# Performance work log

Measured on AMD Instinct MI355X. Metric: run time of the kernel, lower is better.

## Reference

```python
import jax, jax.numpy as jnp
import numpy as np

B, T, D_MODEL, HEAD_DIM = 4, 4096, 1024, 64

def setup_inputs() -> dict:
    key = jax.random.key(0)
    ks = jax.random.split(key, 7)
    s = 1.0 / np.sqrt(D_MODEL)
    return {
        "x": jax.random.normal(ks[0], (B, T, D_MODEL), dtype=jnp.float32),
        "Wq": jax.random.uniform(ks[1], (D_MODEL, HEAD_DIM), jnp.float32, -s, s),
        "bq": jax.random.uniform(ks[2], (HEAD_DIM,), jnp.float32, -s, s),
        "Wk": jax.random.uniform(ks[3], (D_MODEL, HEAD_DIM), jnp.float32, -s, s),
        "bk": jax.random.uniform(ks[4], (HEAD_DIM,), jnp.float32, -s, s),
        "Wv": jax.random.uniform(ks[5], (D_MODEL, HEAD_DIM), jnp.float32, -s, s),
        "bv": jax.random.uniform(ks[6], (HEAD_DIM,), jnp.float32, -s, s),
    }

def reference(x, Wq, bq, Wk, bk, Wv, bv):
    # x: [B,T,D]; projections -> [B,T,H]
    q = jnp.einsum("btd,dh->bth", x, Wq) + bq
    k = jnp.einsum("btd,dh->bth", x, Wk) + bk
    v = jnp.einsum("btd,dh->bth", x, Wv) + bv
    scale = HEAD_DIM ** -0.5
    # scores: [B,Tq,Tk] -- naive full attention matrix (memory-bound)
    scores = jnp.einsum("bqh,bkh->bqk", q, k) * scale
    neg = jnp.finfo(scores.dtype).min
    T_ = scores.shape[-1]
    causal = jnp.triu(jnp.full((T_, T_), neg, dtype=scores.dtype), k=1)
    scores = scores + causal[None, :, :]
    probs = jax.nn.softmax(scores, axis=-1)
    y = jnp.einsum("bqk,bkh->bqh", probs, v)
    return y
```

## Files before the change

kernel.cpp:

```cpp
#include <hip/hip_runtime.h>
#include <hip/hip_bf16.h>

typedef __attribute__((ext_vector_type(4))) float f4v;
typedef __attribute__((ext_vector_type(16))) float f16v;
typedef __attribute__((ext_vector_type(4))) unsigned short u16x4;
typedef __attribute__((ext_vector_type(8))) unsigned short u16x8;
typedef __attribute__((ext_vector_type(2))) unsigned int u32x2;
typedef __attribute__((ext_vector_type(4))) unsigned int u32x4;
typedef __attribute__((ext_vector_type(8))) __bf16 bf16x8;

#define D_MODEL 1024
#define HDIM 64
#define TSEQ 4096
#define QB 32
#define KVB 64
#define QSCALE 0.18033688011112042f

__device__ __forceinline__ unsigned short f2bf(float f) {
    union { float f; unsigned u; } v; v.f = f;
    unsigned r = v.u + 0x7FFFu + ((v.u >> 16) & 1u);
    return (unsigned short)(r >> 16);
}
__device__ __forceinline__ float asf(unsigned u) {
    union { unsigned u; float f; } v; v.u = u; return v.f;
}
__device__ __forceinline__ bf16x8 ld8(const unsigned short* p) {
    return __builtin_bit_cast(bf16x8, *(const u16x8*)p);
}
__device__ __forceinline__ f4v mfma16(bf16x8 a, bf16x8 b, f4v c) {
    return __builtin_amdgcn_mfma_f32_16x16x32_bf16(a, b, c, 0, 0, 0);
}
__device__ __forceinline__ f16v mfma32(bf16x8 a, bf16x8 b, f16v c) {
    return __builtin_amdgcn_mfma_f32_32x32x16_bf16(a, b, c, 0, 0, 0);
}
__device__ __forceinline__ unsigned cvtpk(float a, float b) {
    unsigned r;
    asm("v_cvt_pk_bf16_f32 %0, %1, %2" : "=v"(r) : "v"(a), "v"(b));
    return r;
}
__device__ __forceinline__ void pswap(unsigned& a, unsigned& b) {
    asm("v_permlane32_swap_b32 %0, %1" : "+v"(a), "+v"(b));
}

__global__ void prep_wf(const float* __restrict__ Wq, const float* __restrict__ Wk,
                        const float* __restrict__ Wv, unsigned short* __restrict__ Wf)
{
    int idx = blockIdx.x * 256 + threadIdx.x;
    int j = idx & 7, lane = (idx >> 3) & 63, nf = (idx >> 9) & 3,
        kstep = (idx >> 11) & 31, m = idx >> 16;
    int k = kstep * 32 + 8 * (lane >> 4) + j;
    int n = nf * 16 + (lane & 15);
    const float* W = (m == 0) ? Wq : (m == 1) ? Wk : Wv;
    Wf[idx] = f2bf(W[k * 64 + n]);
}

__global__ __launch_bounds__(256, 2)
void proj_qkv(const float* __restrict__ x, const unsigned short* __restrict__ Wf,
              const float* __restrict__ bq, const float* __restrict__ bk,
              const float* __restrict__ bv,
              unsigned short* __restrict__ Qf, unsigned short* __restrict__ Kf,
              unsigned short* __restrict__ Vf)
{
    __shared__ unsigned short xhi[32][72];
    __shared__ unsigned short xlo[32][72];

    const int tid = threadIdx.x;
    const int w = tid >> 6, l = tid & 63;
    const int row0 = blockIdx.x * 32;

    f4v acc[2][3];
#pragma unroll
    for (int s = 0; s < 2; ++s)
#pragma unroll
        for (int f = 0; f < 3; ++f) acc[s][f] = (f4v)0.f;

    for (int k0 = 0; k0 < D_MODEL; k0 += 64) {
        __syncthreads();
#pragma unroll
        for (int io = 0; io < 2; ++io) {
            int id = io * 256 + tid;
            int r = id >> 4, c4 = id & 15;
            f4v a = *(const f4v*)(x + (size_t)(row0 + r) * D_MODEL + k0 + c4 * 4);
            unsigned p0 = cvtpk(a[0], a[1]), p1 = cvtpk(a[2], a[3]);
            u32x2 hw = {p0, p1};
            *(u16x4*)&xhi[r][c4 * 4] = __builtin_bit_cast(u16x4, hw);
            float e0 = a[0] - asf(p0 << 16), e1 = a[1] - asf(p0 & 0xFFFF0000u);
            float e2 = a[2] - asf(p1 << 16), e3 = a[3] - asf(p1 & 0xFFFF0000u);
            unsigned q0 = cvtpk(e0, e1), q1 = cvtpk(e2, e3);
            u32x2 lw = {q0, q1};
            *(u16x4*)&xlo[r][c4 * 4] = __builtin_bit_cast(u16x4, lw);
        }
        __syncthreads();
#pragma unroll
        for (int ks = 0; ks < 2; ++ks) {
            const int kglob = (k0 >> 5) + ks;
            bf16x8 bw[3];
#pragma unroll
            for (int f = 0; f < 3; ++f) {
                const int cf = w * 3 + f;
                bw[f] = ld8(Wf + ((((cf >> 2) * 32 + kglob) * 4 + (cf & 3)) << 9) + l * 8);
            }
#pragma unroll
            for (int s = 0; s < 2; ++s) {
                bf16x8 xh = ld8(&xhi[s * 16 + (l & 15)][ks * 32 + 8 * (l >> 4)]);
                bf16x8 xl = ld8(&xlo[s * 16 + (l & 15)][ks * 32 + 8 * (l >> 4)]);
#pragma unroll
                for (int f = 0; f < 3; ++f) {
                    acc[s][f] = mfma16(xh, bw[f], acc[s][f]);
                    acc[s][f] = mfma16(xl, bw[f], acc[s][f]);
                }
            }
        }
    }

    const float* bias[3] = {bq, bk, bv};
#pragma unroll
    for (int s = 0; s < 2; ++s) {
        const int rowb = row0 + s * 16 + 4 * (l >> 4);
        const int b = rowb >> 12, tok0 = rowb & 4095;
#pragma unroll
        for (int f = 0; f < 3; ++f) {
            const int cf = w * 3 + f;
            const int m = cf >> 2, nf = cf & 3;
            const int d = nf * 16 + (l & 15);
            const float bb = bias[m][d];
            if (m == 0) {
                const int qtile = tok0 >> 5;
                const int ksq = d >> 4, hq = (d >> 3) & 1, jq = d & 7;
#pragma unroll
                for (int r4 = 0; r4 < 4; ++r4) {
                    int cq = (tok0 & 31) + r4;
                    Qf[(((size_t)(b * 128 + qtile) * 4 + ksq) << 9) + (32 * hq + cq) * 8 + jq] =
                        f2bf((acc[s][f][r4] + bb) * QSCALE);
                }
            } else if (m == 1) {
                const int t = tok0 >> 6, tb = (tok0 >> 5) & 1;
                const int ksk = d >> 4, hk = (d >> 3) & 1, jk = d & 7;
#pragma unroll
                for (int r4 = 0; r4 < 4; ++r4) {
                    int ck = (tok0 & 31) + r4;
                    Kf[(((size_t)((b * 64 + t) * 8 + tb * 4 + ksk)) << 9) + (32 * hk + ck) * 8 + jk] =
                        f2bf(acc[s][f][r4] + bb);
                }
            } else {
                const int t = tok0 >> 6, ku = (tok0 >> 4) & 3, hv = (tok0 >> 3) & 1, jv = tok0 & 7;
                const int cv = d & 31, td = d >> 5;
                u16x4 pk;
#pragma unroll
                for (int r4 = 0; r4 < 4; ++r4) pk[r4] = f2bf(acc[s][f][r4] + bb);
                *(u16x4*)(Vf + (((size_t)((b * 64 + t) * 8 + td * 4 + ku)) << 9) +
                          (32 * hv + cv) * 8 + jv) = pk;
            }
        }
    }
}

struct TState { float m, l; f16v o0, o1; };

__device__ __forceinline__ void run_tile(const unsigned short* __restrict__ Qf,
                                         const unsigned short* __restrict__ Kf,
                                         const unsigned short* __restrict__ Vf,
                                         int batch, int qt, int g8, int l, int h, int c,
                                         TState& st)
{
    const int NT = (qt >> 1) + 1;
    st.m = -1e30f; st.l = 0.f; st.o0 = (f16v)0.f; st.o1 = (f16v)0.f;

    bf16x8 qf[4];
    const unsigned short* qp = Qf + (((size_t)(batch * 128 + qt) * 4) << 9) + l * 8;
#pragma unroll
    for (int ks = 0; ks < 4; ++ks) qf[ks] = ld8(qp + (ks << 9));

    if (g8 >= NT) return;

    auto kload = [&](bf16x8(&kr)[2][4], int t_) {
        const unsigned short* p = Kf + (((size_t)(batch * 64 + t_) * 8) << 9) + l * 8;
#pragma unroll
        for (int tb = 0; tb < 2; ++tb)
#pragma unroll
            for (int ks = 0; ks < 4; ++ks)
                kr[tb][ks] = ld8(p + ((tb * 4 + ks) << 9));
    };

    auto body = [&](bf16x8(&kr)[2][4], bf16x8(&kn)[2][4], int t_) {
        bf16x8 vr[2][4];
        {
            const unsigned short* p = Vf + (((size_t)(batch * 64 + t_) * 8) << 9) + l * 8;
#pragma unroll
            for (int td = 0; td < 2; ++td)
#pragma unroll
                for (int ku = 0; ku < 4; ++ku)
                    vr[td][ku] = ld8(p + ((td * 4 + ku) << 9));
        }
        f16v sacc[2];
        sacc[0] = (f16v)0.f; sacc[1] = (f16v)0.f;
#pragma unroll
        for (int ks = 0; ks < 4; ++ks) {
            sacc[0] = mfma32(kr[0][ks], qf[ks], sacc[0]);
            sacc[1] = mfma32(kr[1][ks], qf[ks], sacc[1]);
        }
        int tn = t_ + 8; if (tn > NT - 1) tn = NT - 1;
        kload(kn, tn);
        if (t_ == NT - 1) {
            const int off = qt * QB - t_ * KVB;
#pragma unroll
            for (int tb = 0; tb < 2; ++tb)
#pragma unroll
                for (int r = 0; r < 16; ++r) {
                    int mv = 32 * tb + (r & 3) + 8 * (r >> 2) + 4 * h - off;
                    if (mv > c) sacc[tb][r] = -1e30f;
                }
        }
        float pm = -1e30f;
#pragma unroll
        for (int tb = 0; tb < 2; ++tb)
#pragma unroll
            for (int r = 0; r < 16; ++r) pm = fmaxf(pm, sacc[tb][r]);
        pm = fmaxf(pm, __shfl_xor(pm, 32));
        const float mnew = fmaxf(st.m, pm);
        const float sc = exp2f(st.m - mnew);
        st.m = mnew;
        float rs = 0.f;
        float p[2][16];
#pragma unroll
        for (int tb = 0; tb < 2; ++tb)
#pragma unroll
            for (int r = 0; r < 16; ++r) {
                float e = exp2f(sacc[tb][r] - mnew);
                p[tb][r] = e; rs += e;
            }
        rs += __shfl_xor(rs, 32);
        st.l = st.l * sc + rs;
#pragma unroll
        for (int r = 0; r < 16; ++r) { st.o0[r] *= sc; st.o1[r] *= sc; }
        bf16x8 pa[4];
#pragma unroll
        for (int tb = 0; tb < 2; ++tb) {
            unsigned wp[8];
#pragma unroll
            for (int i = 0; i < 8; ++i) wp[i] = cvtpk(p[tb][2 * i], p[tb][2 * i + 1]);
            pswap(wp[0], wp[2]); pswap(wp[1], wp[3]);
            pswap(wp[4], wp[6]); pswap(wp[5], wp[7]);
            u32x4 f0 = {wp[0], wp[1], wp[2], wp[3]};
            u32x4 f1 = {wp[4], wp[5], wp[6], wp[7]};
            pa[2 * tb]     = __builtin_bit_cast(bf16x8, f0);
            pa[2 * tb + 1] = __builtin_bit_cast(bf16x8, f1);
        }
#pragma unroll
        for (int ku = 0; ku < 4; ++ku) {
            st.o0 = mfma32(vr[0][ku], pa[ku], st.o0);
            st.o1 = mfma32(vr[1][ku], pa[ku], st.o1);
        }
    };

    bf16x8 kA[2][4], kB[2][4];
    int t = g8;
    kload(kA, t);
    for (;;) {
        body(kA, kB, t);
        t += 8; if (t >= NT) break;
        body(kB, kA, t);
        t += 8; if (t >= NT) break;
    }
}

__global__ __launch_bounds__(512, 2)
void attn(const unsigned short* __restrict__ Qf, const unsigned short* __restrict__ Kf,
          const unsigned short* __restrict__ Vf, float* __restrict__ Yg)
{
    __shared__ float Osm[8][QB][33];
    __shared__ float Msm[2][8][QB];
    __shared__ float Lsm[2][8][QB];

    const int tid = threadIdx.x;
    const int g8 = tid >> 6, l = tid & 63, h = l >> 5, c = l & 31;
    const int batch = blockIdx.x & 3;
    const int pr = blockIdx.x >> 2;
    const int qtA = pr, qtB = 127 - pr;

    TState sB, sA;
    run_tile(Qf, Kf, Vf, batch, qtB, g8, l, h, c, sB);
    run_tile(Qf, Kf, Vf, batch, qtA, g8, l, h, c, sA);

    if (h == 0) {
        Msm[0][g8][c] = sA.m; Lsm[0][g8][c] = sA.l;
        Msm[1][g8][c] = sB.m; Lsm[1][g8][c] = sB.l;
    }

    auto write_partial = [&](const f16v& o) {
#pragma unroll
        for (int r = 0; r < 16; ++r) {
            int dd = (r & 3) + 8 * (r >> 2) + 4 * h;
            Osm[g8][c][dd] = o[r];
        }
    };
    auto merge_phase = [&](int tile, int dhalf, int qt_) {
        const int q = tid >> 4, d2 = (tid & 15) * 2;
        float mm = -1e30f;
#pragma unroll
        for (int gg = 0; gg < 8; ++gg) mm = fmaxf(mm, Msm[tile][gg][q]);
        float L = 0.f, o0 = 0.f, o1 = 0.f;
#pragma unroll
        for (int gg = 0; gg < 8; ++gg) {
            float a = exp2f(Msm[tile][gg][q] - mm);
            L += a * Lsm[tile][gg][q];
            o0 += a * Osm[gg][q][d2];
            o1 += a * Osm[gg][q][d2 + 1];
        }
        float inv = 1.f / L;
        float* yp = Yg + ((size_t)batch * TSEQ + (size_t)qt_ * QB + q) * HDIM + dhalf * 32 + d2;
        yp[0] = o0 * inv; yp[1] = o1 * inv;
    };

    write_partial(sA.o0);
    __syncthreads();
    merge_phase(0, 0, qtA);
    __syncthreads();
    write_partial(sA.o1);
    __syncthreads();
    merge_phase(0, 1, qtA);
    __syncthreads();
    write_partial(sB.o0);
    __syncthreads();
    merge_phase(1, 0, qtB);
    __syncthreads();
    write_partial(sB.o1);
    __syncthreads();
    merge_phase(1, 1, qtB);
}

extern "C" void kernel_launch(void* const* d_in, const int* in_sizes, int n_in,
                              void* d_out, int out_size, void* d_ws, size_t ws_size,
                              hipStream_t stream)
{
    const float* x  = (const float*)d_in[0];
    const float* Wq = (const float*)d_in[1];
    const float* bq = (const float*)d_in[2];
    const float* Wk = (const float*)d_in[3];
    const float* bk = (const float*)d_in[4];
    const float* Wv = (const float*)d_in[5];
    const float* bv = (const float*)d_in[6];
    float* y = (float*)d_out;

    unsigned short* Qb = (unsigned short*)d_ws;
    unsigned short* Kb = Qb + (size_t)1048576;
    unsigned short* Vb = Kb + (size_t)1048576;
    unsigned short* Wf = Vb + (size_t)1048576;

    prep_wf<<<768, 256, 0, stream>>>(Wq, Wk, Wv, Wf);
    proj_qkv<<<512, 256, 0, stream>>>(x, Wf, bq, bk, bv, Qb, Kb, Vb);
    attn<<<256, 512, 0, stream>>>(Qb, Kb, Vb, y);
}
```

Before: 56.76 us.

## Halve projection row tile, double-buffer x staging with register prefetch

```diff
diff --git a/kernel.cpp b/kernel.cpp
--- a/kernel.cpp
+++ b/kernel.cpp
@@ -54,103 +54,94 @@
     Wf[idx] = f2bf(W[k * 64 + n]);
 }
 
-__global__ __launch_bounds__(256, 2)
+__global__ __launch_bounds__(256, 4)
 void proj_qkv(const float* __restrict__ x, const unsigned short* __restrict__ Wf,
               const float* __restrict__ bq, const float* __restrict__ bk,
               const float* __restrict__ bv,
               unsigned short* __restrict__ Qf, unsigned short* __restrict__ Kf,
               unsigned short* __restrict__ Vf)
 {
-    __shared__ unsigned short xhi[32][72];
-    __shared__ unsigned short xlo[32][72];
+    __shared__ unsigned short xhi[2][16][72];
+    __shared__ unsigned short xlo[2][16][72];
 
     const int tid = threadIdx.x;
     const int w = tid >> 6, l = tid & 63;
-    const int row0 = blockIdx.x * 32;
-
-    f4v acc[2][3];
-#pragma unroll
-    for (int s = 0; s < 2; ++s)
-#pragma unroll
-        for (int f = 0; f < 3; ++f) acc[s][f] = (f4v)0.f;
-
-    for (int k0 = 0; k0 < D_MODEL; k0 += 64) {
+    const int row0 = blockIdx.x * 16;
+    const int sr = tid >> 4, sc = tid & 15;
+    const float* xp = x + (size_t)(row0 + sr) * D_MODEL + sc * 4;
+
+    f4v acc[3];
+#pragma unroll
+    for (int f = 0; f < 3; ++f) acc[f] = (f4v)0.f;
+
+    f4v xv = *(const f4v*)xp;
+
+#pragma unroll
+    for (int t = 0; t < 16; ++t) {
+        unsigned p0 = cvtpk(xv[0], xv[1]), p1 = cvtpk(xv[2], xv[3]);
+        u32x2 hw = {p0, p1};
+        *(u16x4*)&xhi[t & 1][sr][sc * 4] = __builtin_bit_cast(u16x4, hw);
+        float e0 = xv[0] - asf(p0 << 16), e1 = xv[1] - asf(p0 & 0xFFFF0000u);
+        float e2 = xv[2] - asf(p1 << 16), e3 = xv[3] - asf(p1 & 0xFFFF0000u);
+        unsigned q0 = cvtpk(e0, e1), q1 = cvtpk(e2, e3);
+        u32x2 lw = {q0, q1};
+        *(u16x4*)&xlo[t & 1][sr][sc * 4] = __builtin_bit_cast(u16x4, lw);
+        if (t < 15) xv = *(const f4v*)(xp + 64 * (t + 1));
         __syncthreads();
 #pragma unroll
-        for (int io = 0; io < 2; ++io) {
-            int id = io * 256 + tid;
-            int r = id >> 4, c4 = id & 15;
-            f4v a = *(const f4v*)(x + (size_t)(row0 + r) * D_MODEL + k0 + c4 * 4);
-            unsigned p0 = cvtpk(a[0], a[1]), p1 = cvtpk(a[2], a[3]);
-            u32x2 hw = {p0, p1};
-            *(u16x4*)&xhi[r][c4 * 4] = __builtin_bit_cast(u16x4, hw);
-            float e0 = a[0] - asf(p0 << 16), e1 = a[1] - asf(p0 & 0xFFFF0000u);
-            float e2 = a[2] - asf(p1 << 16), e3 = a[3] - asf(p1 & 0xFFFF0000u);
-            unsigned q0 = cvtpk(e0, e1), q1 = cvtpk(e2, e3);
-            u32x2 lw = {q0, q1};
-            *(u16x4*)&xlo[r][c4 * 4] = __builtin_bit_cast(u16x4, lw);
-        }
-        __syncthreads();
-#pragma unroll
         for (int ks = 0; ks < 2; ++ks) {
-            const int kglob = (k0 >> 5) + ks;
+            const int kglob = t * 2 + ks;
             bf16x8 bw[3];
 #pragma unroll
             for (int f = 0; f < 3; ++f) {
                 const int cf = w * 3 + f;
                 bw[f] = ld8(Wf + ((((cf >> 2) * 32 + kglob) * 4 + (cf & 3)) << 9) + l * 8);
             }
-#pragma unroll
-            for (int s = 0; s < 2; ++s) {
-                bf16x8 xh = ld8(&xhi[s * 16 + (l & 15)][ks * 32 + 8 * (l >> 4)]);
-                bf16x8 xl = ld8(&xlo[s * 16 + (l & 15)][ks * 32 + 8 * (l >> 4)]);
-#pragma unroll
-                for (int f = 0; f < 3; ++f) {
-                    acc[s][f] = mfma16(xh, bw[f], acc[s][f]);
-                    acc[s][f] = mfma16(xl, bw[f], acc[s][f]);
-                }
+            bf16x8 xh = ld8(&xhi[t & 1][l & 15][ks * 32 + 8 * (l >> 4)]);
+            bf16x8 xl = ld8(&xlo[t & 1][l & 15][ks * 32 + 8 * (l >> 4)]);
+#pragma unroll
+            for (int f = 0; f < 3; ++f) {
+                acc[f] = mfma16(xh, bw[f], acc[f]);
+                acc[f] = mfma16(xl, bw[f], acc[f]);
             }
         }
     }
 
     const float* bias[3] = {bq, bk, bv};
-#pragma unroll
-    for (int s = 0; s < 2; ++s) {
-        const int rowb = row0 + s * 16 + 4 * (l >> 4);
-        const int b = rowb >> 12, tok0 = rowb & 4095;
-#pragma unroll
-        for (int f = 0; f < 3; ++f) {
-            const int cf = w * 3 + f;
-            const int m = cf >> 2, nf = cf & 3;
-            const int d = nf * 16 + (l & 15);
-            const float bb = bias[m][d];
-            if (m == 0) {
-                const int qtile = tok0 >> 5;
-                const int ksq = d >> 4, hq = (d >> 3) & 1, jq = d & 7;
-#pragma unroll
-                for (int r4 = 0; r4 < 4; ++r4) {
-                    int cq = (tok0 & 31) + r4;
-                    Qf[(((size_t)(b * 128 + qtile) * 4 + ksq) << 9) + (32 * hq + cq) * 8 + jq] =
-                        f2bf((acc[s][f][r4] + bb) * QSCALE);
-                }
-            } else if (m == 1) {
-                const int t = tok0 >> 6, tb = (tok0 >> 5) & 1;
-                const int ksk = d >> 4, hk = (d >> 3) & 1, jk = d & 7;
-#pragma unroll
-                for (int r4 = 0; r4 < 4; ++r4) {
-                    int ck = (tok0 & 31) + r4;
-                    Kf[(((size_t)((b * 64 + t) * 8 + tb * 4 + ksk)) << 9) + (32 * hk + ck) * 8 + jk] =
-                        f2bf(acc[s][f][r4] + bb);
-                }
-            } else {
-                const int t = tok0 >> 6, ku = (tok0 >> 4) & 3, hv = (tok0 >> 3) & 1, jv = tok0 & 7;
-                const int cv = d & 31, td = d >> 5;
-                u16x4 pk;
-#pragma unroll
-                for (int r4 = 0; r4 < 4; ++r4) pk[r4] = f2bf(acc[s][f][r4] + bb);
-                *(u16x4*)(Vf + (((size_t)((b * 64 + t) * 8 + td * 4 + ku)) << 9) +
-                          (32 * hv + cv) * 8 + jv) = pk;
-            }
+    const int rowb = row0 + 4 * (l >> 4);
+    const int b = rowb >> 12, tok0 = rowb & 4095;
+#pragma unroll
+    for (int f = 0; f < 3; ++f) {
+        const int cf = w * 3 + f;
+        const int m = cf >> 2, nf = cf & 3;
+        const int d = nf * 16 + (l & 15);
+        const float bb = bias[m][d];
+        if (m == 0) {
+            const int qtile = tok0 >> 5;
+            const int ksq = d >> 4, hq = (d >> 3) & 1, jq = d & 7;
+#pragma unroll
+            for (int r4 = 0; r4 < 4; ++r4) {
+                int cq = (tok0 & 31) + r4;
+                Qf[(((size_t)(b * 128 + qtile) * 4 + ksq) << 9) + (32 * hq + cq) * 8 + jq] =
+                    f2bf((acc[f][r4] + bb) * QSCALE);
+            }
+        } else if (m == 1) {
+            const int t = tok0 >> 6, tb = (tok0 >> 5) & 1;
+            const int ksk = d >> 4, hk = (d >> 3) & 1, jk = d & 7;
+#pragma unroll
+            for (int r4 = 0; r4 < 4; ++r4) {
+                int ck = (tok0 & 31) + r4;
+                Kf[(((size_t)((b * 64 + t) * 8 + tb * 4 + ksk)) << 9) + (32 * hk + ck) * 8 + jk] =
+                    f2bf(acc[f][r4] + bb);
+            }
+        } else {
+            const int t = tok0 >> 6, ku = (tok0 >> 4) & 3, hv = (tok0 >> 3) & 1, jv = tok0 & 7;
+            const int cv = d & 31, td = d >> 5;
+            u16x4 pk;
+#pragma unroll
+            for (int r4 = 0; r4 < 4; ++r4) pk[r4] = f2bf(acc[f][r4] + bb);
+            *(u16x4*)(Vf + (((size_t)((b * 64 + t) * 8 + td * 4 + ku)) << 9) +
+                      (32 * hv + cv) * 8 + jv) = pk;
         }
     }
 }
@@ -348,6 +339,6 @@
     unsigned short* Wf = Vb + (size_t)1048576;
 
     prep_wf<<<768, 256, 0, stream>>>(Wq, Wk, Wv, Wf);
-    proj_qkv<<<512, 256, 0, stream>>>(x, Wf, bq, bk, bv, Qb, Kb, Vb);
+    proj_qkv<<<1024, 256, 0, stream>>>(x, Wf, bq, bk, bv, Qb, Kb, Vb);
     attn<<<256, 512, 0, stream>>>(Qb, Kb, Vb, y);
 }
```

Result: faster. 51.80 us (-8.7%).

## Switch QKV projection to fp16 MFMA with async double-buffered LDS staging

Applied to the files above, without the earlier changes.

```diff
diff --git a/kernel.cpp b/kernel.cpp
--- a/kernel.cpp
+++ b/kernel.cpp
@@ -8,6 +8,7 @@
 typedef __attribute__((ext_vector_type(2))) unsigned int u32x2;
 typedef __attribute__((ext_vector_type(4))) unsigned int u32x4;
 typedef __attribute__((ext_vector_type(8))) __bf16 bf16x8;
+typedef __attribute__((ext_vector_type(8))) _Float16 h8v;
 
 #define D_MODEL 1024
 #define HDIM 64
@@ -21,14 +22,14 @@
     unsigned r = v.u + 0x7FFFu + ((v.u >> 16) & 1u);
     return (unsigned short)(r >> 16);
 }
-__device__ __forceinline__ float asf(unsigned u) {
-    union { unsigned u; float f; } v; v.u = u; return v.f;
-}
 __device__ __forceinline__ bf16x8 ld8(const unsigned short* p) {
     return __builtin_bit_cast(bf16x8, *(const u16x8*)p);
 }
-__device__ __forceinline__ f4v mfma16(bf16x8 a, bf16x8 b, f4v c) {
-    return __builtin_amdgcn_mfma_f32_16x16x32_bf16(a, b, c, 0, 0, 0);
+__device__ __forceinline__ h8v ldh8(const unsigned short* p) {
+    return __builtin_bit_cast(h8v, *(const u16x8*)p);
+}
+__device__ __forceinline__ f4v mfma16f(h8v a, h8v b, f4v c) {
+    return __builtin_amdgcn_mfma_f32_16x16x32_f16(a, b, c, 0, 0, 0);
 }
 __device__ __forceinline__ f16v mfma32(bf16x8 a, bf16x8 b, f16v c) {
     return __builtin_amdgcn_mfma_f32_32x32x16_bf16(a, b, c, 0, 0, 0);
@@ -40,6 +41,14 @@
 }
 __device__ __forceinline__ void pswap(unsigned& a, unsigned& b) {
     asm("v_permlane32_swap_b32 %0, %1" : "+v"(a), "+v"(b));
+}
+__device__ __forceinline__ h8v pack8(f4v a, f4v b) {
+    unsigned p0 = __builtin_bit_cast(unsigned, __builtin_amdgcn_cvt_pkrtz(a[0], a[1]));
+    unsigned p1 = __builtin_bit_cast(unsigned, __builtin_amdgcn_cvt_pkrtz(a[2], a[3]));
+    unsigned p2 = __builtin_bit_cast(unsigned, __builtin_amdgcn_cvt_pkrtz(b[0], b[1]));
+    unsigned p3 = __builtin_bit_cast(unsigned, __builtin_amdgcn_cvt_pkrtz(b[2], b[3]));
+    u32x4 u = {p0, p1, p2, p3};
+    return __builtin_bit_cast(h8v, u);
 }
 
 __global__ void prep_wf(const float* __restrict__ Wq, const float* __restrict__ Wk,
@@ -51,7 +60,8 @@
     int k = kstep * 32 + 8 * (lane >> 4) + j;
     int n = nf * 16 + (lane & 15);
     const float* W = (m == 0) ? Wq : (m == 1) ? Wk : Wv;
-    Wf[idx] = f2bf(W[k * 64 + n]);
+    _Float16 hv = (_Float16)W[k * 64 + n];
+    Wf[idx] = __builtin_bit_cast(unsigned short, hv);
 }
 
 __global__ __launch_bounds__(256, 2)
@@ -61,8 +71,7 @@
               unsigned short* __restrict__ Qf, unsigned short* __restrict__ Kf,
               unsigned short* __restrict__ Vf)
 {
-    __shared__ unsigned short xhi[32][72];
-    __shared__ unsigned short xlo[32][72];
+    __shared__ float xs[2][4096];
 
     const int tid = threadIdx.x;
     const int w = tid >> 6, l = tid & 63;
@@ -74,43 +83,51 @@
 #pragma unroll
         for (int f = 0; f < 3; ++f) acc[s][f] = (f4v)0.f;
 
-    for (int k0 = 0; k0 < D_MODEL; k0 += 64) {
-        __syncthreads();
-#pragma unroll
-        for (int io = 0; io < 2; ++io) {
-            int id = io * 256 + tid;
-            int r = id >> 4, c4 = id & 15;
-            f4v a = *(const f4v*)(x + (size_t)(row0 + r) * D_MODEL + k0 + c4 * 4);
-            unsigned p0 = cvtpk(a[0], a[1]), p1 = cvtpk(a[2], a[3]);
-            u32x2 hw = {p0, p1};
-            *(u16x4*)&xhi[r][c4 * 4] = __builtin_bit_cast(u16x4, hw);
-            float e0 = a[0] - asf(p0 << 16), e1 = a[1] - asf(p0 & 0xFFFF0000u);
-            float e2 = a[2] - asf(p1 << 16), e3 = a[3] - asf(p1 & 0xFFFF0000u);
-            unsigned q0 = cvtpk(e0, e1), q1 = cvtpk(e2, e3);
-            u32x2 lw = {q0, q1};
-            *(u16x4*)&xlo[r][c4 * 4] = __builtin_bit_cast(u16x4, lw);
-        }
-        __syncthreads();
-#pragma unroll
-        for (int ks = 0; ks < 2; ++ks) {
-            const int kglob = (k0 >> 5) + ks;
-            bf16x8 bw[3];
+    auto stage = [&](int buf, int t) {
+#pragma unroll
+        for (int i = 0; i < 4; ++i) {
+            const int G0 = (i * 4 + w) * 64;
+            const int G = G0 + l;
+            const int row = G >> 5;
+            const int gl = (G & 31) ^ (row & 7);
+            const float* src = x + (size_t)(row0 + row) * D_MODEL + t * 128 + gl * 4;
+            __builtin_amdgcn_global_load_lds(
+                (const __attribute__((address_space(1))) unsigned*)src,
+                (__attribute__((address_space(3))) unsigned*)&xs[buf][G0 * 4],
+                16, 0, 0);
+        }
+    };
+
+    stage(0, 0);
+    __syncthreads();
+
+#pragma unroll
+    for (int t = 0; t < 8; ++t) {
+        if (t < 7) stage((t + 1) & 1, t + 1);
+        const int b = t & 1;
+#pragma unroll
+        for (int ks = 0; ks < 4; ++ks) {
+            const int kglob = t * 4 + ks;
+            h8v bw[3];
 #pragma unroll
             for (int f = 0; f < 3; ++f) {
                 const int cf = w * 3 + f;
-                bw[f] = ld8(Wf + ((((cf >> 2) * 32 + kglob) * 4 + (cf & 3)) << 9) + l * 8);
+                bw[f] = ldh8(Wf + ((((cf >> 2) * 32 + kglob) * 4 + (cf & 3)) << 9) + l * 8);
             }
+            const int sw = l & 7;
+            const int gr = ks * 8 + 2 * (l >> 4);
 #pragma unroll
             for (int s = 0; s < 2; ++s) {
-                bf16x8 xh = ld8(&xhi[s * 16 + (l & 15)][ks * 32 + 8 * (l >> 4)]);
-                bf16x8 xl = ld8(&xlo[s * 16 + (l & 15)][ks * 32 + 8 * (l >> 4)]);
-#pragma unroll
-                for (int f = 0; f < 3; ++f) {
-                    acc[s][f] = mfma16(xh, bw[f], acc[s][f]);
-                    acc[s][f] = mfma16(xl, bw[f], acc[s][f]);
-                }
+                const int row = s * 16 + (l & 15);
+                f4v a0 = *(const f4v*)&xs[b][row * 128 + ((gr ^ sw) << 2)];
+                f4v a1 = *(const f4v*)&xs[b][row * 128 + (((gr + 1) ^ sw) << 2)];
+                h8v xa = pack8(a0, a1);
+#pragma unroll
+                for (int f = 0; f < 3; ++f)
+                    acc[s][f] = mfma16f(xa, bw[f], acc[s][f]);
             }
         }
+        __syncthreads();
     }
 
     const float* bias[3] = {bq, bk, bv};
```

After: 52.21 us. 8.0% less time.
